# Kernel optimization log

Measured on AMD Instinct MI355X. Metric: run time of the kernel, lower is better.

The kernel has to match this reference:

```python
import jax, jax.numpy as jnp
import numpy as np

B, N, U = 8, 2048, 256
BN_EPS = 1e-3  # keras BatchNormalization default epsilon
ADJ_DENSITY = 0.008  # ~16 neighbors per node on average


def setup_inputs() -> dict:
    key = jax.random.key(0)
    ks = jax.random.split(key, 16)
    s = 0.05  # weight scale ('random_normal' init is small-stddev in keras)
    x = jax.random.normal(ks[0], (B, N, U), jnp.float32)
    # sparse binary adjacency stored dense (per-sample SpMM pattern)
    adj = (jax.random.uniform(ks[1], (B, N, N)) < ADJ_DENSITY).astype(jnp.float32)
    nodal_mask = jnp.ones((B, N), jnp.float32)
    return {
        'x': x, 'adj': adj, 'nodal_mask': nodal_mask,
        'W_lin': jax.random.normal(ks[2], (U, U)) * s, 'b_lin': jnp.zeros((U,)),
        'Wq_mp': jax.random.normal(ks[3], (3, U, U)) * s, 'bq_mp': jnp.zeros((3, U)),
        'Wk_mp': jax.random.normal(ks[4], (3, U, U)) * s, 'bk_mp': jnp.zeros((3, U)),
        'Wv_mp': jax.random.normal(ks[5], (3, U, U)) * s, 'bv_mp': jnp.zeros((3, U)),
        'Wk_att': jax.random.normal(ks[6], (U, U)) * s,
        'Wv_att': jax.random.normal(ks[7], (U, U)) * s,
        'Wq_att': jax.random.normal(ks[8], (U, U)) * s,
        'Wo_att': jax.random.normal(ks[9], (U, U)) * s,
        'bn_gamma': jnp.ones((U,)), 'bn_beta': jnp.zeros((U,)),
        'bn_mean': jnp.zeros((U,)), 'bn_var': jnp.ones((U,)),
        'W_proj': jax.random.normal(ks[10], (U, U)) * s, 'b_proj': jnp.zeros((U,)),
        'W_res': jax.random.normal(ks[11], (U, U)) * s, 'b_res': jnp.zeros((U,)),
    }


def _dympn(x, adj, Ws, bs, mask):
    # 3 message-passing layers, each applied K_l=2 times (inference value)
    for i in range(3):
        for _ in range(2):
            xn = jnp.einsum('bmn,bnd->bmd', adj, x)  # batched SpMM (graph_conv mode)
            x = jax.nn.silu(jnp.einsum('bmd,de->bme', xn, Ws[i]) + bs[i])
    return x * mask[:, :, None]


def reference(x, adj, nodal_mask, W_lin, b_lin, Wq_mp, bq_mp, Wk_mp, bk_mp,
              Wv_mp, bv_mp, Wk_att, Wv_att, Wq_att, Wo_att,
              bn_gamma, bn_beta, bn_mean, bn_var, W_proj, b_proj, W_res, b_res):
    initial_x = x
    adj = jax.lax.stop_gradient(adj)
    h = jnp.einsum('bnd,de->bne', x, W_lin) + b_lin
    q = _dympn(h, adj, Wq_mp, bq_mp, nodal_mask)
    k = _dympn(h, adj, Wk_mp, bk_mp, nodal_mask)
    v = _dympn(h, adj, Wv_mp, bv_mp, nodal_mask)
    # linear attention
    m = nodal_mask[:, :, None]
    pk = jax.nn.silu(jnp.einsum('bnd,de->bne', k, Wk_att) * m)
    pv = jnp.einsum('bnd,de->bne', v, Wv_att) * m
    pq = jnp.einsum('bnd,de->bne', q, Wq_att)
    kv = jnp.einsum('bnd,bne->bde', pk, pv)       # [B,U,U]
    attn = jnp.einsum('bnd,bde->bne', pq, kv)
    attn = jnp.einsum('bnd,de->bne', attn, Wo_att)
    # batch norm (inference: moving stats) over last axis
    y = attn + initial_x
    y = bn_gamma * (y - bn_mean) * jax.lax.rsqrt(bn_var + BN_EPS) + bn_beta
    out = jax.nn.silu(jnp.einsum('bnd,de->bne', y, W_proj) + b_proj)
    out = out + jnp.einsum('bnd,de->bne', initial_x, W_res) + b_res
    out = out * nodal_mask[:, :, None]
    return out
```

## Files before the change

kernel.cpp:

```cpp
#include <hip/hip_runtime.h>
#include <stdint.h>

#define NB 8
#define NN 2048
#define NU 256
#define CAP 64
#define BNEPS 0.001f

typedef __attribute__((ext_vector_type(8))) short short8;
typedef __attribute__((ext_vector_type(4))) float floatx4;
typedef unsigned short u16;
typedef unsigned int u32;

__device__ __forceinline__ float bf2f(u16 u) {
  union { u32 i; float f; } c; c.i = ((u32)u) << 16; return c.f;
}
__device__ __forceinline__ u16 f2bf(float f) {
  union { float f; u32 i; } c; c.f = f;
  return (u16)((c.i + 0x7fffu + ((c.i >> 16) & 1u)) >> 16);
}
__device__ __forceinline__ void splitbf(float a, u16& h, u16& l) {
  h = f2bf(a);
  l = f2bf(a - bf2f(h));
}

enum : unsigned {
  F_BIAS = 2u, F_SILU = 4u, F_MASKPRE = 8u, F_MASKPOST = 16u,
  F_ADDX = 32u, F_BN = 64u, F_ADDT = 128u, F_BPERMAT = 512u,
  F_TPLANES = 1024u, F_OUTHL = 2048u
};

#define TP_MAT 524288
#define TP_LO  4194304
#define MSZ ((size_t)NN * NU)

struct WPtrs { const float* p[16]; };

__global__ __launch_bounds__(256) void prologue_k(
    WPtrs wp, u16* __restrict__ wdst,
    const float* __restrict__ x, u16* __restrict__ xdst, size_t xLo,
    const float* __restrict__ adj, int* __restrict__ cnt, int* __restrict__ idx)
{
  int bid = blockIdx.x;
  int tid = threadIdx.x;
  __shared__ int c0;
  if (bid < 512) {
    int gid = bid * 256 + tid;
    int mat = gid >> 13;
    int rem = gid & 8191;
    int kb = rem >> 10;
    int n = (rem >> 2) & 255;
    int slot = rem & 3;
    int qv = (slot - (n >> 1)) & 3;
    int k0 = kb * 32 + qv * 8;
    const float* W = wp.p[mat];
    u32 oh[4], ol[4];
#pragma unroll
    for (int t2 = 0; t2 < 4; t2++) {
      float f0 = W[(size_t)(k0 + 2 * t2) * 256 + n];
      float f1 = W[(size_t)(k0 + 2 * t2 + 1) * 256 + n];
      u16 h0, l0, h1, l1;
      splitbf(f0, h0, l0);
      splitbf(f1, h1, l1);
      oh[t2] = (u32)h0 | ((u32)h1 << 16);
      ol[t2] = (u32)l0 | ((u32)l1 << 16);
    }
    uint4 qh; qh.x = oh[0]; qh.y = oh[1]; qh.z = oh[2]; qh.w = oh[3];
    uint4 ql; ql.x = ol[0]; ql.y = ol[1]; ql.z = ol[2]; ql.w = ol[3];
    *(uint4*)(wdst + (size_t)gid * 8) = qh;
    *(uint4*)(wdst + 1048576 + (size_t)gid * 8) = ql;
  } else if (bid < 4608) {
    size_t i = ((size_t)(bid - 512) * 256 + tid) * 4;
    float4 v = *(const float4*)(x + i);
    u16 h0, l0, h1, l1, h2, l2, h3, l3;
    splitbf(v.x, h0, l0); splitbf(v.y, h1, l1);
    splitbf(v.z, h2, l2); splitbf(v.w, h3, l3);
    uint2 H; H.x = (u32)h0 | ((u32)h1 << 16); H.y = (u32)h2 | ((u32)h3 << 16);
    uint2 L; L.x = (u32)l0 | ((u32)l1 << 16); L.y = (u32)l2 | ((u32)l3 << 16);
    *(uint2*)(xdst + i) = H;
    *(uint2*)(xdst + xLo + i) = L;
  } else {
    int row = bid - 4608;
    const float* base = adj + (size_t)row * NN;
    if (tid == 0) c0 = 0;
    __syncthreads();
#pragma unroll
    for (int j = 0; j < 8; j++) {
      int n = j * 256 + tid;
      if (base[n] != 0.f) {
        int p = atomicAdd(&c0, 1);
        if (p < CAP) idx[(size_t)row * CAP + p] = n;
      }
    }
    __syncthreads();
    if (tid == 0) cnt[row] = (c0 < CAP ? c0 : CAP);
  }
}

template <unsigned F>
__device__ __forceinline__ void gemm_epi(
    floatx4 (&acc)[4][2], int b, int bm, int w, int m16, int q,
    const float* __restrict__ bias, const float* __restrict__ mask,
    const float* __restrict__ xf32,
    const float* __restrict__ gma, const float* __restrict__ bta,
    const float* __restrict__ bmu, const float* __restrict__ bvr,
    const float* __restrict__ addt, void* __restrict__ outp, size_t oLo)
{
#pragma unroll
  for (int mt = 0; mt < 4; mt++) {
    if (F & F_TPLANES) {
      u16* oh = (u16*)outp + (size_t)b * TP_MAT;
      u16* ol = oh + TP_LO;
      int gr0 = bm + mt * 16 + q * 4;
#pragma unroll
      for (int nt = 0; nt < 2; nt++) {
        int col = w * 32 + nt * 16 + m16;
        u16 hh[4], ll[4];
#pragma unroll
        for (int r = 0; r < 4; r++) {
          float t2 = acc[mt][nt][r];
          float mv = mask[b * NN + gr0 + r];
          if (F & F_MASKPRE) t2 *= mv;
          if (F & F_SILU) t2 = t2 / (1.f + __expf(-t2));
          if (F & F_MASKPOST) t2 *= mv;
          splitbf(t2, hh[r], ll[r]);
        }
        uint2 H2, L2v;
        H2.x = (u32)hh[0] | ((u32)hh[1] << 16);
        H2.y = (u32)hh[2] | ((u32)hh[3] << 16);
        L2v.x = (u32)ll[0] | ((u32)ll[1] << 16);
        L2v.y = (u32)ll[2] | ((u32)ll[3] << 16);
        *(uint2*)(oh + (size_t)col * 2048 + gr0) = H2;
        *(uint2*)(ol + (size_t)col * 2048 + gr0) = L2v;
      }
    } else {
#pragma unroll
      for (int r = 0; r < 4; r++) {
        int gr = bm + mt * 16 + q * 4 + r;
        float mval = 1.f;
        if (F & (F_MASKPRE | F_MASKPOST)) mval = mask[b * NN + gr];
#pragma unroll
        for (int nt = 0; nt < 2; nt++) {
          int col = w * 32 + nt * 16 + m16;
          float t2 = acc[mt][nt][r];
          if (F & F_BIAS) t2 += bias[col];
          if (F & F_MASKPRE) t2 *= mval;
          if (F & F_SILU) t2 = t2 / (1.f + __expf(-t2));
          if (F & F_ADDX) t2 += xf32[((size_t)b * NN + gr) * NU + col];
          if (F & F_BN) t2 = gma[col] * (t2 - bmu[col]) * rsqrtf(bvr[col] + BNEPS) + bta[col];
          if (F & F_ADDT) t2 += addt[((size_t)b * NN + gr) * NU + col];
          if (F & F_MASKPOST) t2 *= mval;
          size_t o = ((size_t)b * NN + gr) * NU + col;
          if (F & F_OUTHL) {
            u16 h0, l0;
            splitbf(t2, h0, l0);
            ((u16*)outp)[o] = h0;
            ((u16*)outp)[o + oLo] = l0;
          } else {
            ((float*)outp)[o] = t2;
          }
        }
      }
    }
  }
}

template <int NG, unsigned SF, unsigned F0, unsigned F1, unsigned F2>
__global__ __launch_bounds__(512, 4) void gemm_k(
    const u16* __restrict__ A0, const u16* __restrict__ A1, const u16* __restrict__ A2,
    size_t aLo,
    const u16* __restrict__ W0, const u16* __restrict__ W1, const u16* __restrict__ W2,
    size_t wLo,
    const float* __restrict__ b0, const float* __restrict__ b1, const float* __restrict__ b2,
    const float* __restrict__ mask,
    const float* __restrict__ xf32,
    const float* __restrict__ gma, const float* __restrict__ bta,
    const float* __restrict__ bmu, const float* __restrict__ bvr,
    const float* __restrict__ addt,
    void* __restrict__ o0, void* __restrict__ o1, void* __restrict__ o2,
    size_t oLo,
    const float* __restrict__ gsrc,
    const float* __restrict__ sb0, const float* __restrict__ sb1, const float* __restrict__ sb2,
    const int* __restrict__ ncnt, const int* __restrict__ nidx)
{
  const int tid = threadIdx.x;
  const int id = blockIdx.x;
  const int xcd = id & 7;
  const int t = id >> 3;
  const int chain = (NG == 1) ? 0 : (t >> 5);
  const int xt = (NG == 1) ? t : (t & 31);
  const int b = xcd;
  const int bm = xt * 64;

  __shared__ alignas(16) u16 Ah[64 * 264];
  __shared__ alignas(16) u16 Al[64 * 264];

  const u16* Wsel = (chain == 0) ? W0 : (chain == 1 ? W1 : W2);
  if (F0 & F_BPERMAT) Wsel = W0 + (size_t)b * 65536;
  const u16* Whi = Wsel;
  const u16* Wlo = Whi + wLo;

  if constexpr (SF != 0u) {
    const int l = tid & 63;
    const int wv = tid >> 6;
    const float* __restrict__ gm = gsrc + ((size_t)chain * 8 + b) * MSZ;
    const float* sb = (chain == 0) ? sb0 : (chain == 1 ? sb1 : sb2);
    const int c = l * 4;
    float4 bb = *(const float4*)(sb + c);
#pragma unroll 1
    for (int i = 0; i < 8; i++) {
      const int r = wv * 8 + i;
      const int gr = bm + r;
      const int rowid = b * NN + gr;
      const int cnt = ncnt[rowid];
      const int* __restrict__ ip = nidx + (size_t)rowid * CAP;
      float4 a; a.x = a.y = a.z = a.w = 0.f;
      int e = 0;
      for (; e + 4 <= cnt; e += 4) {
        int4 i4 = *(const int4*)(ip + e);
        float4 v0 = *(const float4*)(gm + ((size_t)i4.x << 8) + c);
        float4 v1 = *(const float4*)(gm + ((size_t)i4.y << 8) + c);
        float4 v2 = *(const float4*)(gm + ((size_t)i4.z << 8) + c);
        float4 v3 = *(const float4*)(gm + ((size_t)i4.w << 8) + c);
        a.x += v0.x + v1.x + v2.x + v3.x;
        a.y += v0.y + v1.y + v2.y + v3.y;
        a.z += v0.z + v1.z + v2.z + v3.z;
        a.w += v0.w + v1.w + v2.w + v3.w;
      }
      for (; e < cnt; e++) {
        float4 v = *(const float4*)(gm + ((size_t)ip[e] << 8) + c);
        a.x += v.x; a.y += v.y; a.z += v.z; a.w += v.w;
      }
      float ov[4] = {a.x + bb.x, a.y + bb.y, a.z + bb.z, a.w + bb.w};
      float mv = (SF & F_MASKPOST) ? mask[rowid] : 1.f;
      u16 hh[4], ll[4];
#pragma unroll
      for (int j = 0; j < 4; j++) {
        float t2 = ov[j];
        if (SF & F_SILU) t2 = t2 / (1.f + __expf(-t2));
        if (SF & F_MASKPOST) t2 *= mv;
        splitbf(t2, hh[j], ll[j]);
      }
      uint2 H; H.x = (u32)hh[0] | ((u32)hh[1] << 16); H.y = (u32)hh[2] | ((u32)hh[3] << 16);
      uint2 L; L.x = (u32)ll[0] | ((u32)ll[1] << 16); L.y = (u32)ll[2] | ((u32)ll[3] << 16);
      *(uint2*)&Ah[r * 264 + c] = H;
      *(uint2*)&Al[r * 264 + c] = L;
    }
  } else {
    const u16* Abase = (chain == 0) ? A0 : (chain == 1 ? A1 : A2);
    const u16* Ahp = Abase + (size_t)b * MSZ;
    const u16* Alp = Ahp + aLo;
#pragma unroll
    for (int s = tid; s < 1024; s += 512) {
      int r = s >> 4;
      int c = (s & 15) << 4;
      size_t ao = (size_t)(bm + r) * 256 + c;
      *(uint4*)&Ah[r * 264 + c] = *(const uint4*)(Ahp + ao);
      *(uint4*)&Ah[r * 264 + c + 8] = *(const uint4*)(Ahp + ao + 8);
      *(uint4*)&Al[r * 264 + c] = *(const uint4*)(Alp + ao);
      *(uint4*)&Al[r * 264 + c + 8] = *(const uint4*)(Alp + ao + 8);
    }
  }
  __syncthreads();

  const int lane = tid & 63;
  const int w = tid >> 6;
  const int m16 = lane & 15;
  const int q = lane >> 4;

  floatx4 acc[4][2];
#pragma unroll
  for (int i = 0; i < 4; i++)
#pragma unroll
    for (int j = 0; j < 2; j++) acc[i][j] = (floatx4){0.f, 0.f, 0.f, 0.f};

#pragma unroll
  for (int kk = 0; kk < 8; kk++) {
    short8 bh[2], bl2[2];
#pragma unroll
    for (int nt = 0; nt < 2; nt++) {
      int n = w * 32 + nt * 16 + m16;
      size_t off = (size_t)kk * 8192 + (size_t)n * 32 + (size_t)(((q + (n >> 1)) & 3) * 8);
      bh[nt] = *(const short8*)(Whi + off);
      bl2[nt] = *(const short8*)(Wlo + off);
    }
#pragma unroll
    for (int mt = 0; mt < 4; mt++) {
      int row = mt * 16 + m16;
      short8 ah = *(const short8*)&Ah[row * 264 + kk * 32 + q * 8];
      short8 al2 = *(const short8*)&Al[row * 264 + kk * 32 + q * 8];
#pragma unroll
      for (int nt = 0; nt < 2; nt++) {
        acc[mt][nt] = __builtin_amdgcn_mfma_f32_16x16x32_bf16(ah, bh[nt], acc[mt][nt], 0, 0, 0);
        acc[mt][nt] = __builtin_amdgcn_mfma_f32_16x16x32_bf16(al2, bh[nt], acc[mt][nt], 0, 0, 0);
        acc[mt][nt] = __builtin_amdgcn_mfma_f32_16x16x32_bf16(ah, bl2[nt], acc[mt][nt], 0, 0, 0);
      }
    }
  }

  if (NG == 1 || chain == 0)
    gemm_epi<F0>(acc, b, bm, w, m16, q, b0, mask, xf32, gma, bta, bmu, bvr, addt, o0, oLo);
  else if (chain == 1)
    gemm_epi<F1>(acc, b, bm, w, m16, q, b1, mask, xf32, gma, bta, bmu, bvr, addt, o1, oLo);
  else
    gemm_epi<F2>(acc, b, bm, w, m16, q, b2, mask, xf32, gma, bta, bmu, bvr, addt, o2, oLo);
}

__global__ __launch_bounds__(256, 2) void kv_k(
    const u16* __restrict__ pkT, const u16* __restrict__ pvT, float* __restrict__ part)
{
  int et = blockIdx.x * 128;
  int dt = blockIdx.y * 128;
  int z = blockIdx.z;
  int b = z & 7;
  int p = z >> 3;
  int tid = threadIdx.x;
  int lane = tid & 63, w = tid >> 6;
  int m16 = lane & 15, q = lane >> 4;

  const u16* pkh = pkT + (size_t)b * TP_MAT;
  const u16* pkl = pkh + TP_LO;
  const u16* pvh = pvT + (size_t)b * TP_MAT;
  const u16* pvl = pvh + TP_LO;

  int d_base = dt + (w >> 1) * 64 + m16;
  int e_base = et + (w & 1) * 64 + m16;

  floatx4 acc[4][4];
#pragma unroll
  for (int i = 0; i < 4; i++)
#pragma unroll
    for (int j = 0; j < 4; j++) acc[i][j] = (floatx4){0.f, 0.f, 0.f, 0.f};

#pragma unroll
  for (int kt = 0; kt < 8; kt++) {
    int kc = p * 256 + kt * 32 + q * 8;
    short8 ah[4], al[4], bh[4], bl[4];
#pragma unroll
    for (int mt = 0; mt < 4; mt++) {
      size_t o = (size_t)(d_base + mt * 16) * 2048 + kc;
      ah[mt] = *(const short8*)(pkh + o);
      al[mt] = *(const short8*)(pkl + o);
    }
#pragma unroll
    for (int nt = 0; nt < 4; nt++) {
      size_t o = (size_t)(e_base + nt * 16) * 2048 + kc;
      bh[nt] = *(const short8*)(pvh + o);
      bl[nt] = *(const short8*)(pvl + o);
    }
#pragma unroll
    for (int mt = 0; mt < 4; mt++)
#pragma unroll
      for (int nt = 0; nt < 4; nt++) {
        acc[mt][nt] = __builtin_amdgcn_mfma_f32_16x16x32_bf16(ah[mt], bh[nt], acc[mt][nt], 0, 0, 0);
        acc[mt][nt] = __builtin_amdgcn_mfma_f32_16x16x32_bf16(al[mt], bh[nt], acc[mt][nt], 0, 0, 0);
        acc[mt][nt] = __builtin_amdgcn_mfma_f32_16x16x32_bf16(ah[mt], bl[nt], acc[mt][nt], 0, 0, 0);
      }
  }

#pragma unroll
  for (int mt = 0; mt < 4; mt++)
#pragma unroll
    for (int r = 0; r < 4; r++) {
      int d = dt + (w >> 1) * 64 + mt * 16 + q * 4 + r;
#pragma unroll
      for (int nt = 0; nt < 4; nt++) {
        int e = et + (w & 1) * 64 + nt * 16 + m16;
        part[(size_t)z * 65536 + (size_t)d * 256 + e] = acc[mt][nt][r];
      }
    }
}

__global__ __launch_bounds__(256) void kv_conv_k(const float* __restrict__ part, u16* __restrict__ dst)
{
  int gid = blockIdx.x * 256 + threadIdx.x;
  int b = gid >> 13;
  int rem = gid & 8191;
  int kb = rem >> 10;
  int e = (rem >> 2) & 255;
  int slot = rem & 3;
  int qv = (slot - (e >> 1)) & 3;
  int d0 = kb * 32 + qv * 8;
  const float* src = part + (size_t)b * 65536 + (size_t)d0 * 256 + e;
  u32 oh[4], ol[4];
#pragma unroll
  for (int t2 = 0; t2 < 4; t2++) {
    float s0 = 0.f, s1 = 0.f;
#pragma unroll
    for (int pp = 0; pp < 8; pp++) {
      const float* sp = src + (size_t)pp * 524288 + t2 * 512;
      s0 += sp[0];
      s1 += sp[256];
    }
    u16 h0, l0, h1, l1;
    splitbf(s0, h0, l0);
    splitbf(s1, h1, l1);
    oh[t2] = (u32)h0 | ((u32)h1 << 16);
    ol[t2] = (u32)l0 | ((u32)l1 << 16);
  }
  uint4 qh; qh.x = oh[0]; qh.y = oh[1]; qh.z = oh[2]; qh.w = oh[3];
  uint4 ql; ql.x = ol[0]; ql.y = ol[1]; ql.z = ol[2]; ql.w = ol[3];
  *(uint4*)(dst + (size_t)gid * 8) = qh;
  *(uint4*)(dst + 524288 + (size_t)gid * 8) = ql;
}

extern "C" void kernel_launch(void* const* d_in, const int* in_sizes, int n_in,
                              void* d_out, int out_size, void* d_ws, size_t ws_size,
                              hipStream_t stream)
{
  const float* x = (const float*)d_in[0];
  const float* adj = (const float*)d_in[1];
  const float* mask = (const float*)d_in[2];
  const float* W_lin = (const float*)d_in[3];
  const float* b_lin = (const float*)d_in[4];
  const float* Wq_mp = (const float*)d_in[5];
  const float* bq_mp = (const float*)d_in[6];
  const float* Wk_mp = (const float*)d_in[7];
  const float* bk_mp = (const float*)d_in[8];
  const float* Wv_mp = (const float*)d_in[9];
  const float* bv_mp = (const float*)d_in[10];
  const float* Wk_att = (const float*)d_in[11];
  const float* Wv_att = (const float*)d_in[12];
  const float* Wq_att = (const float*)d_in[13];
  const float* Wo_att = (const float*)d_in[14];
  const float* bn_gamma = (const float*)d_in[15];
  const float* bn_beta = (const float*)d_in[16];
  const float* bn_mean = (const float*)d_in[17];
  const float* bn_var = (const float*)d_in[18];
  const float* W_proj = (const float*)d_in[19];
  const float* b_proj = (const float*)d_in[20];
  const float* W_res = (const float*)d_in[21];
  const float* b_res = (const float*)d_in[22];

  char* ws = (char*)d_ws;
  int* CNT    = (int*)(ws + 0);
  int* IDX    = (int*)(ws + (1ull << 20));
  u16* WSZ    = (u16*)(ws + (5ull << 20));
  u16* KVS    = (u16*)(ws + (9ull << 20));
  float* KVP  = (float*)(ws + (11ull << 20));
  u16* XHL    = (u16*)(ws + (27ull << 20));
  u16* HHL    = (u16*)(ws + (43ull << 20));
  float* GA   = (float*)(ws + (59ull << 20));
  float* GB   = (float*)(ws + (107ull << 20));
  u16* PKT    = (u16*)(ws + (155ull << 20));
  u16* PVT    = (u16*)(ws + (171ull << 20));
  u16* ATT    = (u16*)(ws + (187ull << 20));
  u16* YHL    = (u16*)(ws + (203ull << 20));
  float* TMP  = (float*)(ws + (219ull << 20));

  const size_t WLO = 1048576;
  const size_t KLO = 524288;
  const size_t A8  = 8 * MSZ;

  u16* PQHL = HHL;

  WPtrs wp;
  wp.p[0] = W_lin;
  wp.p[1] = Wq_mp; wp.p[2] = Wq_mp + 65536; wp.p[3] = Wq_mp + 131072;
  wp.p[4] = Wk_mp; wp.p[5] = Wk_mp + 65536; wp.p[6] = Wk_mp + 131072;
  wp.p[7] = Wv_mp; wp.p[8] = Wv_mp + 65536; wp.p[9] = Wv_mp + 131072;
  wp.p[10] = Wk_att; wp.p[11] = Wv_att; wp.p[12] = Wq_att; wp.p[13] = Wo_att;
  wp.p[14] = W_proj; wp.p[15] = W_res;
  prologue_k<<<20992, 256, 0, stream>>>(wp, WSZ, x, XHL, A8, adj, CNT, IDX);

  gemm_k<1, 0u, F_BIAS | F_OUTHL, 0u, 0u><<<256, 512, 0, stream>>>(
      XHL, XHL, XHL, A8, WSZ, WSZ, WSZ, WLO,
      b_lin, nullptr, nullptr, mask, nullptr,
      bn_gamma, bn_beta, bn_mean, bn_var, nullptr,
      HHL, nullptr, nullptr, A8,
      nullptr, nullptr, nullptr, nullptr, CNT, IDX);

  gemm_k<3, 0u, 0u, 0u, 0u><<<768, 512, 0, stream>>>(
      HHL, HHL, HHL, A8,
      WSZ + (size_t)1 * 65536, WSZ + (size_t)4 * 65536, WSZ + (size_t)7 * 65536, WLO,
      nullptr, nullptr, nullptr, mask, nullptr,
      bn_gamma, bn_beta, bn_mean, bn_var, nullptr,
      GA, GA + 8 * MSZ, GA + 16 * MSZ, 0,
      nullptr, nullptr, nullptr, nullptr, CNT, IDX);

  for (int s = 1; s < 6; s++) {
    int iw = s >> 1;
    int ib = (s - 1) >> 1;
    float* Gin = (s & 1) ? GA : GB;
    float* Gout = (s & 1) ? GB : GA;
    gemm_k<3, F_BIAS | F_SILU, 0u, 0u, 0u><<<768, 512, 0, stream>>>(
        nullptr, nullptr, nullptr, 0,
        WSZ + (size_t)(1 + iw) * 65536, WSZ + (size_t)(4 + iw) * 65536,
        WSZ + (size_t)(7 + iw) * 65536, WLO,
        nullptr, nullptr, nullptr, mask, nullptr,
        bn_gamma, bn_beta, bn_mean, bn_var, nullptr,
        Gout, Gout + 8 * MSZ, Gout + 16 * MSZ, 0,
        Gin, bq_mp + ib * 256, bk_mp + ib * 256, bv_mp + ib * 256, CNT, IDX);
  }

  gemm_k<3, F_BIAS | F_SILU | F_MASKPOST,
         F_OUTHL, F_SILU | F_MASKPRE | F_TPLANES, F_MASKPOST | F_TPLANES>
      <<<768, 512, 0, stream>>>(
      nullptr, nullptr, nullptr, 0,
      WSZ + (size_t)12 * 65536, WSZ + (size_t)10 * 65536, WSZ + (size_t)11 * 65536, WLO,
      nullptr, nullptr, nullptr, mask, nullptr,
      bn_gamma, bn_beta, bn_mean, bn_var, nullptr,
      PQHL, PKT, PVT, A8,
      GB, bq_mp + 512, bk_mp + 512, bv_mp + 512, CNT, IDX);

  kv_k<<<dim3(2, 2, 64), 256, 0, stream>>>(PKT, PVT, KVP);
  kv_conv_k<<<256, 256, 0, stream>>>(KVP, KVS);

  gemm_k<1, 0u, F_BPERMAT | F_OUTHL, 0u, 0u><<<256, 512, 0, stream>>>(
      PQHL, PQHL, PQHL, A8, KVS, KVS, KVS, KLO,
      nullptr, nullptr, nullptr, mask, nullptr,
      bn_gamma, bn_beta, bn_mean, bn_var, nullptr,
      ATT, nullptr, nullptr, A8,
      nullptr, nullptr, nullptr, nullptr, CNT, IDX);

  gemm_k<1, 0u, F_ADDX | F_BN | F_OUTHL, 0u, 0u><<<256, 512, 0, stream>>>(
      ATT, ATT, ATT, A8,
      WSZ + (size_t)13 * 65536, nullptr, nullptr, WLO,
      nullptr, nullptr, nullptr, mask, x,
      bn_gamma, bn_beta, bn_mean, bn_var, nullptr,
      YHL, nullptr, nullptr, A8,
      nullptr, nullptr, nullptr, nullptr, CNT, IDX);

  gemm_k<1, 0u, F_BIAS, 0u, 0u><<<256, 512, 0, stream>>>(
      XHL, XHL, XHL, A8,
      WSZ + (size_t)15 * 65536, nullptr, nullptr, WLO,
      b_res, nullptr, nullptr, mask, nullptr,
      bn_gamma, bn_beta, bn_mean, bn_var, nullptr,
      TMP, nullptr, nullptr, 0,
      nullptr, nullptr, nullptr, nullptr, CNT, IDX);

  gemm_k<1, 0u, F_BIAS | F_SILU | F_ADDT | F_MASKPOST, 0u, 0u><<<256, 512, 0, stream>>>(
      YHL, YHL, YHL, A8,
      WSZ + (size_t)14 * 65536, nullptr, nullptr, WLO,
      b_proj, nullptr, nullptr, mask, nullptr,
      bn_gamma, bn_beta, bn_mean, bn_var, TMP,
      d_out, nullptr, nullptr, 0,
      nullptr, nullptr, nullptr, nullptr, CNT, IDX);

  (void)in_sizes; (void)n_in; (void)out_size; (void)ws_size;
}
```

Measured before the change: 840.9 us.

## Halve GEMM row tile, interleave SpMM gathers, fuse final projection and residual GEMMs

Shrinks each GEMM block from 64 to 32 rows, which doubles grid sizes and raises the launch-bounds occupancy target to 8 blocks per CU. The neighbor-gather SpMM now processes 4 rows per wave in an interleaved loop, so more independent loads are in flight at once. The final W_proj and W_res GEMMs are fused into one kernel: it applies silu to the projection accumulator, reloads the x tile into shared memory and accumulates the residual GEMM on top. This removes a launch and the fp32 TMP round trip. In exchange, each block reloads weights for only half as many rows, which lowers weight reuse.

```diff
diff --git a/kernel.cpp b/kernel.cpp
--- a/kernel.cpp
+++ b/kernel.cpp
@@ -99,7 +99,7 @@
 
 template <unsigned F>
 __device__ __forceinline__ void gemm_epi(
-    floatx4 (&acc)[4][2], int b, int bm, int w, int m16, int q,
+    floatx4 (&acc)[2][2], int b, int bm, int w, int m16, int q,
     const float* __restrict__ bias, const float* __restrict__ mask,
     const float* __restrict__ xf32,
     const float* __restrict__ gma, const float* __restrict__ bta,
@@ -107,7 +107,7 @@
     const float* __restrict__ addt, void* __restrict__ outp, size_t oLo)
 {
 #pragma unroll
-  for (int mt = 0; mt < 4; mt++) {
+  for (int mt = 0; mt < 2; mt++) {
     if (F & F_TPLANES) {
       u16* oh = (u16*)outp + (size_t)b * TP_MAT;
       u16* ol = oh + TP_LO;
@@ -165,8 +165,8 @@
   }
 }
 
-template <int NG, unsigned SF, unsigned F0, unsigned F1, unsigned F2>
-__global__ __launch_bounds__(512, 4) void gemm_k(
+template <int NG, unsigned SF, unsigned F0, unsigned F1, unsigned F2, bool DK = false>
+__global__ __launch_bounds__(512, 8) void gemm_k(
     const u16* __restrict__ A0, const u16* __restrict__ A1, const u16* __restrict__ A2,
     size_t aLo,
     const u16* __restrict__ W0, const u16* __restrict__ W1, const u16* __restrict__ W2,
@@ -187,52 +187,70 @@
   const int id = blockIdx.x;
   const int xcd = id & 7;
   const int t = id >> 3;
-  const int chain = (NG == 1) ? 0 : (t >> 5);
-  const int xt = (NG == 1) ? t : (t & 31);
+  const int chain = (NG == 1) ? 0 : (t >> 6);
+  const int xt = (NG == 1) ? t : (t & 63);
   const int b = xcd;
-  const int bm = xt * 64;
-
-  __shared__ alignas(16) u16 Ah[64 * 264];
-  __shared__ alignas(16) u16 Al[64 * 264];
+  const int bm = xt * 32;
+
+  __shared__ alignas(16) u16 Ah[32 * 264];
+  __shared__ alignas(16) u16 Al[32 * 264];
 
   const u16* Wsel = (chain == 0) ? W0 : (chain == 1 ? W1 : W2);
   if (F0 & F_BPERMAT) Wsel = W0 + (size_t)b * 65536;
   const u16* Whi = Wsel;
   const u16* Wlo = Whi + wLo;
 
+  const int lane = tid & 63;
+  const int w = tid >> 6;
+
   if constexpr (SF != 0u) {
-    const int l = tid & 63;
-    const int wv = tid >> 6;
     const float* __restrict__ gm = gsrc + ((size_t)chain * 8 + b) * MSZ;
     const float* sb = (chain == 0) ? sb0 : (chain == 1 ? sb1 : sb2);
-    const int c = l * 4;
+    const int c = lane * 4;
     float4 bb = *(const float4*)(sb + c);
-#pragma unroll 1
-    for (int i = 0; i < 8; i++) {
-      const int r = wv * 8 + i;
-      const int gr = bm + r;
-      const int rowid = b * NN + gr;
-      const int cnt = ncnt[rowid];
-      const int* __restrict__ ip = nidx + (size_t)rowid * CAP;
-      float4 a; a.x = a.y = a.z = a.w = 0.f;
-      int e = 0;
-      for (; e + 4 <= cnt; e += 4) {
-        int4 i4 = *(const int4*)(ip + e);
-        float4 v0 = *(const float4*)(gm + ((size_t)i4.x << 8) + c);
-        float4 v1 = *(const float4*)(gm + ((size_t)i4.y << 8) + c);
-        float4 v2 = *(const float4*)(gm + ((size_t)i4.z << 8) + c);
-        float4 v3 = *(const float4*)(gm + ((size_t)i4.w << 8) + c);
-        a.x += v0.x + v1.x + v2.x + v3.x;
-        a.y += v0.y + v1.y + v2.y + v3.y;
-        a.z += v0.z + v1.z + v2.z + v3.z;
-        a.w += v0.w + v1.w + v2.w + v3.w;
-      }
-      for (; e < cnt; e++) {
-        float4 v = *(const float4*)(gm + ((size_t)ip[e] << 8) + c);
-        a.x += v.x; a.y += v.y; a.z += v.z; a.w += v.w;
-      }
-      float ov[4] = {a.x + bb.x, a.y + bb.y, a.z + bb.z, a.w + bb.w};
-      float mv = (SF & F_MASKPOST) ? mask[rowid] : 1.f;
+    const int r0 = w * 4;
+    int cnts[4];
+    const int* ips[4];
+    float4 av[4];
+    int rowids[4];
+#pragma unroll
+    for (int i = 0; i < 4; i++) {
+      rowids[i] = b * NN + bm + r0 + i;
+      cnts[i] = ncnt[rowids[i]];
+      ips[i] = nidx + (size_t)rowids[i] * CAP;
+      av[i].x = av[i].y = av[i].z = av[i].w = 0.f;
+    }
+    int maxc = cnts[0];
+    maxc = cnts[1] > maxc ? cnts[1] : maxc;
+    maxc = cnts[2] > maxc ? cnts[2] : maxc;
+    maxc = cnts[3] > maxc ? cnts[3] : maxc;
+    for (int e = 0; e + 4 <= maxc; e += 4) {
+#pragma unroll
+      for (int i = 0; i < 4; i++) {
+        if (e + 4 <= cnts[i]) {
+          int4 i4 = *(const int4*)(ips[i] + e);
+          float4 v0 = *(const float4*)(gm + ((size_t)i4.x << 8) + c);
+          float4 v1 = *(const float4*)(gm + ((size_t)i4.y << 8) + c);
+          float4 v2 = *(const float4*)(gm + ((size_t)i4.z << 8) + c);
+          float4 v3 = *(const float4*)(gm + ((size_t)i4.w << 8) + c);
+          av[i].x += v0.x + v1.x + v2.x + v3.x;
+          av[i].y += v0.y + v1.y + v2.y + v3.y;
+          av[i].z += v0.z + v1.z + v2.z + v3.z;
+          av[i].w += v0.w + v1.w + v2.w + v3.w;
+        }
+      }
+    }
+#pragma unroll
+    for (int i = 0; i < 4; i++) {
+      for (int e = cnts[i] & ~3; e < cnts[i]; e++) {
+        float4 v = *(const float4*)(gm + ((size_t)ips[i][e] << 8) + c);
+        av[i].x += v.x; av[i].y += v.y; av[i].z += v.z; av[i].w += v.w;
+      }
+    }
+#pragma unroll
+    for (int i = 0; i < 4; i++) {
+      float ov[4] = {av[i].x + bb.x, av[i].y + bb.y, av[i].z + bb.z, av[i].w + bb.w};
+      float mv = (SF & F_MASKPOST) ? mask[rowids[i]] : 1.f;
       u16 hh[4], ll[4];
 #pragma unroll
       for (int j = 0; j < 4; j++) {
@@ -243,15 +261,15 @@
       }
       uint2 H; H.x = (u32)hh[0] | ((u32)hh[1] << 16); H.y = (u32)hh[2] | ((u32)hh[3] << 16);
       uint2 L; L.x = (u32)ll[0] | ((u32)ll[1] << 16); L.y = (u32)ll[2] | ((u32)ll[3] << 16);
-      *(uint2*)&Ah[r * 264 + c] = H;
-      *(uint2*)&Al[r * 264 + c] = L;
+      *(uint2*)&Ah[(r0 + i) * 264 + c] = H;
+      *(uint2*)&Al[(r0 + i) * 264 + c] = L;
     }
   } else {
     const u16* Abase = (chain == 0) ? A0 : (chain == 1 ? A1 : A2);
     const u16* Ahp = Abase + (size_t)b * MSZ;
     const u16* Alp = Ahp + aLo;
-#pragma unroll
-    for (int s = tid; s < 1024; s += 512) {
+    {
+      int s = tid;
       int r = s >> 4;
       int c = (s & 15) << 4;
       size_t ao = (size_t)(bm + r) * 256 + c;
@@ -263,14 +281,12 @@
   }
   __syncthreads();
 
-  const int lane = tid & 63;
-  const int w = tid >> 6;
   const int m16 = lane & 15;
   const int q = lane >> 4;
 
-  floatx4 acc[4][2];
-#pragma unroll
-  for (int i = 0; i < 4; i++)
+  floatx4 acc[2][2];
+#pragma unroll
+  for (int i = 0; i < 2; i++)
 #pragma unroll
     for (int j = 0; j < 2; j++) acc[i][j] = (floatx4){0.f, 0.f, 0.f, 0.f};
 
@@ -285,7 +301,7 @@
       bl2[nt] = *(const short8*)(Wlo + off);
     }
 #pragma unroll
-    for (int mt = 0; mt < 4; mt++) {
+    for (int mt = 0; mt < 2; mt++) {
       int row = mt * 16 + m16;
       short8 ah = *(const short8*)&Ah[row * 264 + kk * 32 + q * 8];
       short8 al2 = *(const short8*)&Al[row * 264 + kk * 32 + q * 8];
@@ -294,6 +310,60 @@
         acc[mt][nt] = __builtin_amdgcn_mfma_f32_16x16x32_bf16(ah, bh[nt], acc[mt][nt], 0, 0, 0);
         acc[mt][nt] = __builtin_amdgcn_mfma_f32_16x16x32_bf16(al2, bh[nt], acc[mt][nt], 0, 0, 0);
         acc[mt][nt] = __builtin_amdgcn_mfma_f32_16x16x32_bf16(ah, bl2[nt], acc[mt][nt], 0, 0, 0);
+      }
+    }
+  }
+
+  if constexpr (DK) {
+#pragma unroll
+    for (int mt = 0; mt < 2; mt++)
+#pragma unroll
+      for (int nt = 0; nt < 2; nt++) {
+        int col = w * 32 + nt * 16 + m16;
+        float bp = b1[col];
+#pragma unroll
+        for (int r = 0; r < 4; r++) {
+          float t2 = acc[mt][nt][r] + bp;
+          acc[mt][nt][r] = t2 / (1.f + __expf(-t2));
+        }
+      }
+    __syncthreads();
+    {
+      const u16* Ahp = A1 + (size_t)b * MSZ;
+      const u16* Alp = Ahp + aLo;
+      int s = tid;
+      int r = s >> 4;
+      int c = (s & 15) << 4;
+      size_t ao = (size_t)(bm + r) * 256 + c;
+      *(uint4*)&Ah[r * 264 + c] = *(const uint4*)(Ahp + ao);
+      *(uint4*)&Ah[r * 264 + c + 8] = *(const uint4*)(Ahp + ao + 8);
+      *(uint4*)&Al[r * 264 + c] = *(const uint4*)(Alp + ao);
+      *(uint4*)&Al[r * 264 + c + 8] = *(const uint4*)(Alp + ao + 8);
+    }
+    __syncthreads();
+    const u16* W1h = W1;
+    const u16* W1l = W1 + wLo;
+#pragma unroll
+    for (int kk = 0; kk < 8; kk++) {
+      short8 bh[2], bl2[2];
+#pragma unroll
+      for (int nt = 0; nt < 2; nt++) {
+        int n = w * 32 + nt * 16 + m16;
+        size_t off = (size_t)kk * 8192 + (size_t)n * 32 + (size_t)(((q + (n >> 1)) & 3) * 8);
+        bh[nt] = *(const short8*)(W1h + off);
+        bl2[nt] = *(const short8*)(W1l + off);
+      }
+#pragma unroll
+      for (int mt = 0; mt < 2; mt++) {
+        int row = mt * 16 + m16;
+        short8 ah = *(const short8*)&Ah[row * 264 + kk * 32 + q * 8];
+        short8 al2 = *(const short8*)&Al[row * 264 + kk * 32 + q * 8];
+#pragma unroll
+        for (int nt = 0; nt < 2; nt++) {
+          acc[mt][nt] = __builtin_amdgcn_mfma_f32_16x16x32_bf16(ah, bh[nt], acc[mt][nt], 0, 0, 0);
+          acc[mt][nt] = __builtin_amdgcn_mfma_f32_16x16x32_bf16(al2, bh[nt], acc[mt][nt], 0, 0, 0);
+          acc[mt][nt] = __builtin_amdgcn_mfma_f32_16x16x32_bf16(ah, bl2[nt], acc[mt][nt], 0, 0, 0);
+        }
       }
     }
   }
@@ -446,7 +516,6 @@
   u16* PVT    = (u16*)(ws + (171ull << 20));
   u16* ATT    = (u16*)(ws + (187ull << 20));
   u16* YHL    = (u16*)(ws + (203ull << 20));
-  float* TMP  = (float*)(ws + (219ull << 20));
 
   const size_t WLO = 1048576;
   const size_t KLO = 524288;
@@ -463,14 +532,14 @@
   wp.p[14] = W_proj; wp.p[15] = W_res;
   prologue_k<<<20992, 256, 0, stream>>>(wp, WSZ, x, XHL, A8, adj, CNT, IDX);
 
-  gemm_k<1, 0u, F_BIAS | F_OUTHL, 0u, 0u><<<256, 512, 0, stream>>>(
+  gemm_k<1, 0u, F_BIAS | F_OUTHL, 0u, 0u><<<512, 512, 0, stream>>>(
       XHL, XHL, XHL, A8, WSZ, WSZ, WSZ, WLO,
       b_lin, nullptr, nullptr, mask, nullptr,
       bn_gamma, bn_beta, bn_mean, bn_var, nullptr,
       HHL, nullptr, nullptr, A8,
       nullptr, nullptr, nullptr, nullptr, CNT, IDX);
 
-  gemm_k<3, 0u, 0u, 0u, 0u><<<768, 512, 0, stream>>>(
+  gemm_k<3, 0u, 0u, 0u, 0u><<<1536, 512, 0, stream>>>(
       HHL, HHL, HHL, A8,
       WSZ + (size_t)1 * 65536, WSZ + (size_t)4 * 65536, WSZ + (size_t)7 * 65536, WLO,
       nullptr, nullptr, nullptr, mask, nullptr,
@@ -483,7 +552,7 @@
     int ib = (s - 1) >> 1;
     float* Gin = (s & 1) ? GA : GB;
     float* Gout = (s & 1) ? GB : GA;
-    gemm_k<3, F_BIAS | F_SILU, 0u, 0u, 0u><<<768, 512, 0, stream>>>(
+    gemm_k<3, F_BIAS | F_SILU, 0u, 0u, 0u><<<1536, 512, 0, stream>>>(
         nullptr, nullptr, nullptr, 0,
         WSZ + (size_t)(1 + iw) * 65536, WSZ + (size_t)(4 + iw) * 65536,
         WSZ + (size_t)(7 + iw) * 65536, WLO,
@@ -495,7 +564,7 @@
 
   gemm_k<3, F_BIAS | F_SILU | F_MASKPOST,
          F_OUTHL, F_SILU | F_MASKPRE | F_TPLANES, F_MASKPOST | F_TPLANES>
-      <<<768, 512, 0, stream>>>(
+      <<<1536, 512, 0, stream>>>(
       nullptr, nullptr, nullptr, 0,
       WSZ + (size_t)12 * 65536, WSZ + (size_t)10 * 65536, WSZ + (size_t)11 * 65536, WLO,
       nullptr, nullptr, nullptr, mask, nullptr,
@@ -506,14 +575,14 @@
   kv_k<<<dim3(2, 2, 64), 256, 0, stream>>>(PKT, PVT, KVP);
   kv_conv_k<<<256, 256, 0, stream>>>(KVP, KVS);
 
-  gemm_k<1, 0u, F_BPERMAT | F_OUTHL, 0u, 0u><<<256, 512, 0, stream>>>(
+  gemm_k<1, 0u, F_BPERMAT | F_OUTHL, 0u, 0u><<<512, 512, 0, stream>>>(
       PQHL, PQHL, PQHL, A8, KVS, KVS, KVS, KLO,
       nullptr, nullptr, nullptr, mask, nullptr,
       bn_gamma, bn_beta, bn_mean, bn_var, nullptr,
       ATT, nullptr, nullptr, A8,
       nullptr, nullptr, nullptr, nullptr, CNT, IDX);
 
-  gemm_k<1, 0u, F_ADDX | F_BN | F_OUTHL, 0u, 0u><<<256, 512, 0, stream>>>(
+  gemm_k<1, 0u, F_ADDX | F_BN | F_OUTHL, 0u, 0u><<<512, 512, 0, stream>>>(
       ATT, ATT, ATT, A8,
       WSZ + (size_t)13 * 65536, nullptr, nullptr, WLO,
       nullptr, nullptr, nullptr, mask, x,
@@ -521,19 +590,11 @@
       YHL, nullptr, nullptr, A8,
       nullptr, nullptr, nullptr, nullptr, CNT, IDX);
 
-  gemm_k<1, 0u, F_BIAS, 0u, 0u><<<256, 512, 0, stream>>>(
-      XHL, XHL, XHL, A8,
-      WSZ + (size_t)15 * 65536, nullptr, nullptr, WLO,
-      b_res, nullptr, nullptr, mask, nullptr,
+  gemm_k<1, 0u, F_BIAS | F_MASKPOST, 0u, 0u, true><<<512, 512, 0, stream>>>(
+      YHL, XHL, YHL, A8,
+      WSZ + (size_t)14 * 65536, WSZ + (size_t)15 * 65536, nullptr, WLO,
+      b_res, b_proj, nullptr, mask, nullptr,
       bn_gamma, bn_beta, bn_mean, bn_var, nullptr,
-      TMP, nullptr, nullptr, 0,
-      nullptr, nullptr, nullptr, nullptr, CNT, IDX);
-
-  gemm_k<1, 0u, F_BIAS | F_SILU | F_ADDT | F_MASKPOST, 0u, 0u><<<256, 512, 0, stream>>>(
-      YHL, YHL, YHL, A8,
-      WSZ + (size_t)14 * 65536, nullptr, nullptr, WLO,
-      b_proj, nullptr, nullptr, mask, nullptr,
-      bn_gamma, bn_beta, bn_mean, bn_var, TMP,
       d_out, nullptr, nullptr, 0,
       nullptr, nullptr, nullptr, nullptr, CNT, IDX);
 
```

Result: faster. 759.3 us (-9.7%).
